# Kernel optimization log

Measured on AMD Instinct MI355X. Metric: run time of the kernel, lower is better.

Reference implementation:

```python
import jax, jax.numpy as jnp
import numpy as np

N_NODES = 100000
N_EDGES = 1600000
IN_DIM = 128
OUT_DIM = 64


def setup_inputs() -> dict:
    key = jax.random.key(0)
    k1, k2, k3 = jax.random.split(key, 3)
    x = jax.random.normal(k1, (N_NODES, IN_DIM), dtype=jnp.float32)
    edge_index = jax.random.randint(k2, (2, N_EDGES), 0, N_NODES, dtype=jnp.int64)
    W = jax.random.normal(k3, (IN_DIM, OUT_DIM), dtype=jnp.float32) * (1.0 / np.sqrt(IN_DIM))
    b = jnp.zeros((OUT_DIM,), dtype=jnp.float32)
    return {"x": x, "edge_index": edge_index, "W": W, "b": b}


def reference(x, edge_index, W, b):
    row = edge_index[0]  # source nodes
    col = edge_index[1]  # target nodes (aggregation index)
    n = x.shape[0]

    # gcn_norm with add_self_loops=False: degree from edge weights (ones) at target
    ones = jnp.ones((edge_index.shape[1],), dtype=x.dtype)
    deg = jax.ops.segment_sum(ones, col, num_segments=n)  # [N]
    deg_inv_sqrt = jnp.where(deg > 0, jax.lax.rsqrt(jnp.maximum(deg, 1e-12)), 0.0)
    norm = deg_inv_sqrt[row] * deg_inv_sqrt[col]  # [E]

    # linear transform first (bias added after aggregation, as in PyG GCNConv)
    h = x @ W  # [N, OUT_DIM]

    # gather source features, scale by norm, scatter-add to targets
    msg = h[row] * norm[:, None]  # [E, OUT_DIM]
    out = jax.ops.segment_sum(msg, col, num_segments=n) + b  # [N, OUT_DIM]

    return jax.nn.relu(out)
```

## Files before the change

kernel.cpp:

```cpp
#include <hip/hip_runtime.h>
#include <hip/hip_bf16.h>

#define IN_DIM 128
#define OUT_DIM 64
#define CLOG 9
#define CNPB (1 << CLOG)
#define FLOG 7
#define FNPB (1 << FLOG)
#define MAXCOARSE 1024
#define B1 256
#define CAP 4096

static inline size_t align_up(size_t v, size_t a) { return (v + a - 1) & ~(a - 1); }

__device__ __forceinline__ unsigned short f2bf(float f) {
    unsigned int x = __float_as_uint(f);
    unsigned int r = (x + 0x7fffu + ((x >> 16) & 1u)) >> 16;
    return (unsigned short)r;
}

typedef _Float16 half8 __attribute__((ext_vector_type(8)));
typedef float f32x4 __attribute__((ext_vector_type(4)));

__global__ void __launch_bounds__(256) kA_ticket(
    const int* __restrict__ col, int* __restrict__ BinTotal,
    int* __restrict__ tickets, int n_edges, int nbuck, int chunk) {
    __shared__ int hist[MAXCOARSE];
    int t = threadIdx.x;
    for (int i = t; i < nbuck; i += 256) hist[i] = 0;
    __syncthreads();
    int start = blockIdx.x * chunk;
    int end = min(n_edges, start + chunk);
    for (int i = start + t; i < end; i += 256)
        atomicAdd(&hist[col[i] >> CLOG], 1);
    __syncthreads();
    int* trow = tickets + (size_t)blockIdx.x * nbuck;
    for (int i = t; i < nbuck; i += 256)
        trow[i] = atomicAdd(&BinTotal[i], hist[i]);
}

__global__ void __launch_bounds__(256) kS2_scantotals(
    const int* __restrict__ BinTotal, int* __restrict__ BucketStart,
    int nbuck, int n_edges) {
    __shared__ int s[256];
    int t = threadIdx.x;
    int v[4];
#pragma unroll
    for (int j = 0; j < 4; ++j) {
        int idx = t * 4 + j;
        v[j] = (idx < nbuck) ? BinTotal[idx] : 0;
    }
    int tsum = v[0] + v[1] + v[2] + v[3];
    s[t] = tsum;
    __syncthreads();
    for (int off = 1; off < 256; off <<= 1) {
        int x = (t >= off) ? s[t - off] : 0;
        __syncthreads();
        s[t] += x;
        __syncthreads();
    }
    int run = s[t] - tsum;
#pragma unroll
    for (int j = 0; j < 4; ++j) {
        int idx = t * 4 + j;
        if (idx < nbuck) BucketStart[idx] = run;
        run += v[j];
    }
    if (t == 0) BucketStart[nbuck] = n_edges;
}

__global__ void __launch_bounds__(256) kB_scatter(
    const int* __restrict__ row, const int* __restrict__ col,
    const int* __restrict__ BucketStart, const int* __restrict__ tickets,
    unsigned int* __restrict__ EdgeBuf, int n_edges, int nbuck, int chunk) {
    __shared__ int cur[MAXCOARSE];
    const int* trow = tickets + (size_t)blockIdx.x * nbuck;
    int t = threadIdx.x;
    for (int i = t; i < nbuck; i += 256)
        cur[i] = BucketStart[i] + trow[i];
    __syncthreads();
    int start = blockIdx.x * chunk;
    int end = min(n_edges, start + chunk);
    for (int i = start + t; i < end; i += 256) {
        int c = col[i];
        int r = row[i];
        int bin = c >> CLOG;
        int p = atomicAdd(&cur[bin], 1);
        EdgeBuf[p] = ((unsigned int)r << CLOG) | (unsigned int)(c & (CNPB - 1));
    }
}

__global__ void __launch_bounds__(256) kD_degree(
    const unsigned int* __restrict__ EdgeBuf, const int* __restrict__ BucketStart,
    float* __restrict__ dis, int n_nodes) {
    __shared__ int cnt[CNPB];
    int t = threadIdx.x;
    for (int i = t; i < CNPB; i += 256) cnt[i] = 0;
    __syncthreads();
    int es = BucketStart[blockIdx.x];
    int ee = BucketStart[blockIdx.x + 1];
    for (int i = es + t; i < ee; i += 256)
        atomicAdd(&cnt[EdgeBuf[i] & (CNPB - 1)], 1);
    __syncthreads();
    int nb0 = blockIdx.x << CLOG;
    for (int i = t; i < CNPB; i += 256) {
        int node = nb0 + i;
        if (node < n_nodes) {
            int d = cnt[i];
            dis[node] = (d > 0) ? rsqrtf((float)d) : 0.0f;
        }
    }
}

__global__ void __launch_bounds__(256) k_matmul_mfma(
    const float* __restrict__ x, const float* __restrict__ W,
    const float* __restrict__ dis, unsigned short* __restrict__ h, int n_nodes) {
    const int lane = threadIdx.x & 63;
    const int m = lane & 15;
    const int q = lane >> 4;
    const int wid = (blockIdx.x * blockDim.x + threadIdx.x) >> 6;
    const int ntiles = (n_nodes + 15) >> 4;
    if (wid >= ntiles) return;

    half8 bfrag[4][4];
#pragma unroll
    for (int kt = 0; kt < 4; ++kt) {
#pragma unroll
        for (int nt = 0; nt < 4; ++nt) {
            int k0 = kt * 32 + q * 8;
            int c = nt * 16 + m;
#pragma unroll
            for (int j = 0; j < 8; ++j)
                bfrag[kt][nt][j] = (_Float16)W[(size_t)(k0 + j) * OUT_DIM + c];
        }
    }

    const int nb = wid << 4;
    int arow = nb + m;
    if (arow >= n_nodes) arow = n_nodes - 1;
    const float* xr = x + (size_t)arow * IN_DIM;

    f32x4 acc[4];
#pragma unroll
    for (int nt = 0; nt < 4; ++nt) acc[nt] = (f32x4){0.f, 0.f, 0.f, 0.f};

#pragma unroll
    for (int kt = 0; kt < 4; ++kt) {
        const float4* xp = (const float4*)(xr + kt * 32 + q * 8);
        float4 lo = xp[0];
        float4 hi = xp[1];
        half8 afrag;
        afrag[0] = (_Float16)lo.x; afrag[1] = (_Float16)lo.y;
        afrag[2] = (_Float16)lo.z; afrag[3] = (_Float16)lo.w;
        afrag[4] = (_Float16)hi.x; afrag[5] = (_Float16)hi.y;
        afrag[6] = (_Float16)hi.z; afrag[7] = (_Float16)hi.w;
#pragma unroll
        for (int nt = 0; nt < 4; ++nt)
            acc[nt] = __builtin_amdgcn_mfma_f32_16x16x32_f16(afrag, bfrag[kt][nt],
                                                             acc[nt], 0, 0, 0);
    }

#pragma unroll
    for (int r = 0; r < 4; ++r) {
        int node = nb + q * 4 + r;
        if (node < n_nodes) {
            float dv = dis[node];
            unsigned short* hp = h + (size_t)node * OUT_DIM + m;
#pragma unroll
            for (int nt = 0; nt < 4; ++nt)
                hp[nt * 16] = f2bf(acc[nt][r] * dv);
        }
    }
}

__global__ void __launch_bounds__(512) kF_sortagg(
    const unsigned int* __restrict__ EdgeBuf, const int* __restrict__ BucketStart,
    const float* __restrict__ dis, const unsigned short* __restrict__ h,
    const float* __restrict__ b, float* __restrict__ out,
    int* __restrict__ spill, int* __restrict__ spillcur, int n_nodes) {
    __shared__ int cnt[FNPB];
    __shared__ int seg[FNPB];
    __shared__ int cursor[FNPB];
    __shared__ int sbuf[CAP];
    __shared__ int sbase_sh;
    int t = threadIdx.x;
    int parent = blockIdx.x >> 2;
    int sub = blockIdx.x & 3;
    int es = BucketStart[parent];
    int ee = BucketStart[parent + 1];
    int nb0 = blockIdx.x << FLOG;

    if (t < FNPB) cnt[t] = 0;
    __syncthreads();
    for (int i = es + t; i < ee; i += 512) {
        unsigned int v = EdgeBuf[i];
        if ((int)((v >> FLOG) & 3u) == sub)
            atomicAdd(&cnt[v & (FNPB - 1)], 1);
    }
    __syncthreads();

    if (t < FNPB) seg[t] = cnt[t];
    __syncthreads();
    for (int off = 1; off < FNPB; off <<= 1) {
        int x = 0;
        if (t < FNPB && t >= off) x = seg[t - off];
        __syncthreads();
        if (t < FNPB) seg[t] += x;
        __syncthreads();
    }
    if (t < FNPB) cursor[t] = seg[t] - cnt[t];
    __syncthreads();

    int ne_f = seg[FNPB - 1];
    if (t == 0 && ne_f > CAP) sbase_sh = atomicAdd(spillcur, ne_f);
    __syncthreads();

    const int lane = t & 63;
    const int wv = t >> 6;
    const int quarter = lane >> 4;
    const int qlane = lane & 15;
    float4 bias = ((const float4*)b)[qlane];

    if (ne_f <= CAP) {
        for (int i = es + t; i < ee; i += 512) {
            unsigned int v = EdgeBuf[i];
            if ((int)((v >> FLOG) & 3u) == sub) {
                int p = atomicAdd(&cursor[v & (FNPB - 1)], 1);
                sbuf[p] = (int)(v >> CLOG);
            }
        }
        __syncthreads();

        for (int nl = wv; nl < FNPB; nl += 8) {
            int node = nb0 + nl;
            if (node >= n_nodes) break;
            int e_ = seg[nl];
            int s_ = e_ - cnt[nl];
            float a0 = 0.f, a1 = 0.f, a2 = 0.f, a3 = 0.f;
            for (int j0 = s_; j0 < e_; j0 += 8) {
                int iA = j0 + quarter;
                int iB = j0 + quarter + 4;
                int rA = sbuf[iA < e_ ? iA : s_];
                int rB = sbuf[iB < e_ ? iB : s_];
                uint2 vA = make_uint2(0u, 0u), vB = make_uint2(0u, 0u);
                if (iA < e_)
                    vA = *(const uint2*)(h + (size_t)rA * OUT_DIM + qlane * 4);
                if (iB < e_)
                    vB = *(const uint2*)(h + (size_t)rB * OUT_DIM + qlane * 4);
                a0 += __uint_as_float(vA.x << 16);
                a1 += __uint_as_float(vA.x & 0xFFFF0000u);
                a2 += __uint_as_float(vA.y << 16);
                a3 += __uint_as_float(vA.y & 0xFFFF0000u);
                a0 += __uint_as_float(vB.x << 16);
                a1 += __uint_as_float(vB.x & 0xFFFF0000u);
                a2 += __uint_as_float(vB.y << 16);
                a3 += __uint_as_float(vB.y & 0xFFFF0000u);
            }
            a0 += __shfl_xor(a0, 16, 64); a0 += __shfl_xor(a0, 32, 64);
            a1 += __shfl_xor(a1, 16, 64); a1 += __shfl_xor(a1, 32, 64);
            a2 += __shfl_xor(a2, 16, 64); a2 += __shfl_xor(a2, 32, 64);
            a3 += __shfl_xor(a3, 16, 64); a3 += __shfl_xor(a3, 32, 64);
            if (quarter == 0) {
                float dv = dis[node];
                float4 o;
                o.x = fmaxf(fmaf(a0, dv, bias.x), 0.f);
                o.y = fmaxf(fmaf(a1, dv, bias.y), 0.f);
                o.z = fmaxf(fmaf(a2, dv, bias.z), 0.f);
                o.w = fmaxf(fmaf(a3, dv, bias.w), 0.f);
                ((float4*)(out + (size_t)node * OUT_DIM))[qlane] = o;
            }
        }
    } else {
        int sbase = sbase_sh;
        for (int i = es + t; i < ee; i += 512) {
            unsigned int v = EdgeBuf[i];
            if ((int)((v >> FLOG) & 3u) == sub) {
                int p = atomicAdd(&cursor[v & (FNPB - 1)], 1);
                spill[sbase + p] = (int)(v >> CLOG);
            }
        }
        __threadfence();
        __syncthreads();
        for (int nl = wv; nl < FNPB; nl += 8) {
            int node = nb0 + nl;
            if (node >= n_nodes) break;
            int e_ = seg[nl];
            int s_ = e_ - cnt[nl];
            float a0 = 0.f, a1 = 0.f, a2 = 0.f, a3 = 0.f;
            for (int j0 = s_; j0 < e_; j0 += 8) {
                int iA = j0 + quarter;
                int iB = j0 + quarter + 4;
                int rA = spill[sbase + (iA < e_ ? iA : s_)];
                int rB = spill[sbase + (iB < e_ ? iB : s_)];
                uint2 vA = make_uint2(0u, 0u), vB = make_uint2(0u, 0u);
                if (iA < e_)
                    vA = *(const uint2*)(h + (size_t)rA * OUT_DIM + qlane * 4);
                if (iB < e_)
                    vB = *(const uint2*)(h + (size_t)rB * OUT_DIM + qlane * 4);
                a0 += __uint_as_float(vA.x << 16);
                a1 += __uint_as_float(vA.x & 0xFFFF0000u);
                a2 += __uint_as_float(vA.y << 16);
                a3 += __uint_as_float(vA.y & 0xFFFF0000u);
                a0 += __uint_as_float(vB.x << 16);
                a1 += __uint_as_float(vB.x & 0xFFFF0000u);
                a2 += __uint_as_float(vB.y << 16);
                a3 += __uint_as_float(vB.y & 0xFFFF0000u);
            }
            a0 += __shfl_xor(a0, 16, 64); a0 += __shfl_xor(a0, 32, 64);
            a1 += __shfl_xor(a1, 16, 64); a1 += __shfl_xor(a1, 32, 64);
            a2 += __shfl_xor(a2, 16, 64); a2 += __shfl_xor(a2, 32, 64);
            a3 += __shfl_xor(a3, 16, 64); a3 += __shfl_xor(a3, 32, 64);
            if (quarter == 0) {
                float dv = dis[node];
                float4 o;
                o.x = fmaxf(fmaf(a0, dv, bias.x), 0.f);
                o.y = fmaxf(fmaf(a1, dv, bias.y), 0.f);
                o.z = fmaxf(fmaf(a2, dv, bias.z), 0.f);
                o.w = fmaxf(fmaf(a3, dv, bias.w), 0.f);
                ((float4*)(out + (size_t)node * OUT_DIM))[qlane] = o;
            }
        }
    }
}

#define MM_NODES 16
__global__ void __launch_bounds__(256) k_matmul_f32(
    const float* __restrict__ x, const float* __restrict__ W,
    const float* __restrict__ dis, float* __restrict__ h, int n_nodes) {
    __shared__ float xs[MM_NODES * IN_DIM];
    const int lane = threadIdx.x & 63;
    const int wv = threadIdx.x >> 6;
    float w[IN_DIM];
#pragma unroll
    for (int k = 0; k < IN_DIM; ++k) w[k] = W[k * OUT_DIM + lane];
    int nchunks = (n_nodes + MM_NODES - 1) / MM_NODES;
    for (int ch = blockIdx.x; ch < nchunks; ch += gridDim.x) {
        int base = ch * MM_NODES;
        int nrows = min(MM_NODES, n_nodes - base);
        __syncthreads();
        const float4* xg = (const float4*)(x + (size_t)base * IN_DIM);
        int nf4 = nrows * IN_DIM / 4;
        for (int i = threadIdx.x; i < nf4; i += 256) ((float4*)xs)[i] = xg[i];
        __syncthreads();
#pragma unroll
        for (int j = 0; j < 4; ++j) {
            int local = wv * 4 + j;
            int node = base + local;
            if (local < nrows) {
                const float4* xr = (const float4*)(xs + local * IN_DIM);
                float acc = 0.0f;
#pragma unroll
                for (int k4 = 0; k4 < IN_DIM / 4; ++k4) {
                    float4 xv = xr[k4];
                    acc = fmaf(xv.x, w[k4 * 4 + 0], acc);
                    acc = fmaf(xv.y, w[k4 * 4 + 1], acc);
                    acc = fmaf(xv.z, w[k4 * 4 + 2], acc);
                    acc = fmaf(xv.w, w[k4 * 4 + 3], acc);
                }
                h[(size_t)node * OUT_DIM + lane] = acc * dis[node];
            }
        }
    }
}

__global__ void k_degree_fb(const int* __restrict__ col, int* __restrict__ deg,
                            int n_edges) {
    int i = blockIdx.x * blockDim.x + threadIdx.x;
    int stride = gridDim.x * blockDim.x;
    for (; i < n_edges; i += stride) atomicAdd(&deg[col[i]], 1);
}

__global__ void k_rsqrt_fb(const int* __restrict__ deg, float* __restrict__ dis, int n) {
    int i = blockIdx.x * blockDim.x + threadIdx.x;
    if (i < n) {
        int d = deg[i];
        dis[i] = (d > 0) ? rsqrtf((float)d) : 0.0f;
    }
}

__global__ void __launch_bounds__(256) k_scatter_fb(
    const int* __restrict__ row, const int* __restrict__ col,
    const float* __restrict__ dis, const float* __restrict__ h,
    float* __restrict__ out, int n_edges) {
    const int lane = threadIdx.x & 63;
    int e = (blockIdx.x * blockDim.x + threadIdx.x) >> 6;
    int nw = (gridDim.x * blockDim.x) >> 6;
    for (; e < n_edges; e += nw) {
        int r = row[e];
        int c = col[e];
        float v = h[(size_t)r * OUT_DIM + lane] * dis[c];
        atomicAdd(&out[(size_t)c * OUT_DIM + lane], v);
    }
}

__global__ void k_bias_relu_fb(float* __restrict__ out, const float* __restrict__ b,
                               int total) {
    int i = blockIdx.x * blockDim.x + threadIdx.x;
    int stride = gridDim.x * blockDim.x;
    for (; i < total; i += stride) {
        float v = out[i] + b[i & (OUT_DIM - 1)];
        out[i] = fmaxf(v, 0.0f);
    }
}

extern "C" void kernel_launch(void* const* d_in, const int* in_sizes, int n_in,
                              void* d_out, int out_size, void* d_ws, size_t ws_size,
                              hipStream_t stream) {
    const float* x = (const float*)d_in[0];
    const int* ei = (const int*)d_in[1];
    const float* W = (const float*)d_in[2];
    const float* b = (const float*)d_in[3];
    float* out = (float*)d_out;

    const int n_nodes = in_sizes[0] / IN_DIM;
    const int n_edges = in_sizes[1] / 2;
    const int* row = ei;
    const int* col = ei + n_edges;

    const int nbc = (n_nodes + CNPB - 1) >> CLOG;
    const int nbf = (n_nodes + FNPB - 1) >> FLOG;
    const int chunk = (n_edges + B1 - 1) / B1;

    char* wsb = (char*)d_ws;
    size_t off = 0;
    int* BinTotal = (int*)(wsb + off);   off += align_up((size_t)(nbc + 8) * 4, 256);
    int* spillcur = BinTotal + nbc;
    int* BucketStart = (int*)(wsb + off);off += align_up((size_t)(nbc + 1) * 4, 256);
    int* tickets = (int*)(wsb + off);    off += align_up((size_t)B1 * nbc * 4, 256);
    float* dis = (float*)(wsb + off);    off += align_up((size_t)n_nodes * 4, 256);
    unsigned int* EdgeBuf = (unsigned int*)(wsb + off);
                                         off += align_up((size_t)n_edges * 4, 256);
    int* spill = (int*)(wsb + off);      off += align_up((size_t)n_edges * 4, 256);
    unsigned short* h = (unsigned short*)(wsb + off);
                                         off += (size_t)n_nodes * OUT_DIM * 2;
    const size_t needed = off;

    const bool ok = (ws_size >= needed) && (nbc <= MAXCOARSE) &&
                    (n_nodes <= (1 << 22));

    if (ok) {
        hipMemsetAsync(BinTotal, 0, (size_t)(nbc + 8) * 4, stream);
        kA_ticket<<<B1, 256, 0, stream>>>(col, BinTotal, tickets, n_edges, nbc,
                                          chunk);
        kS2_scantotals<<<1, 256, 0, stream>>>(BinTotal, BucketStart, nbc, n_edges);
        kB_scatter<<<B1, 256, 0, stream>>>(row, col, BucketStart, tickets, EdgeBuf,
                                           n_edges, nbc, chunk);
        kD_degree<<<nbc, 256, 0, stream>>>(EdgeBuf, BucketStart, dis, n_nodes);
        int ntiles = (n_nodes + 15) / 16;
        int mm_blocks = (ntiles + 3) / 4;
        k_matmul_mfma<<<mm_blocks, 256, 0, stream>>>(x, W, dis, h, n_nodes);
        kF_sortagg<<<nbf, 512, 0, stream>>>(EdgeBuf, BucketStart, dis, h, b,
                                            out, spill, spillcur, n_nodes);
    } else {
        char* p = (char*)d_ws;
        int* deg_f = (int*)p;
        float* dis_f = (float*)(p + align_up((size_t)n_nodes * 4, 256));
        float* h_f = (float*)(p + 2 * align_up((size_t)n_nodes * 4, 256));
        hipMemsetAsync(deg_f, 0, (size_t)n_nodes * 4, stream);
        hipMemsetAsync(out, 0, (size_t)out_size * 4, stream);
        k_degree_fb<<<1024, 256, 0, stream>>>(col, deg_f, n_edges);
        k_rsqrt_fb<<<(n_nodes + 255) / 256, 256, 0, stream>>>(deg_f, dis_f, n_nodes);
        k_matmul_f32<<<1024, 256, 0, stream>>>(x, W, dis_f, h_f, n_nodes);
        k_scatter_fb<<<2048, 256, 0, stream>>>(row, col, dis_f, h_f, out, n_edges);
        k_bias_relu_fb<<<2048, 256, 0, stream>>>(out, b, n_nodes * OUT_DIM);
    }
}
```

Before: 193.3 us.

## Fuse edge bucketing passes into one cooperative kernel with fine buckets

Replaces the ticket/scan/scatter/degree kernel sequence with a single cooperative kernel that uses grid-wide syncs, keeping per-block bucket offsets in shared memory instead of a global tickets array. It also switches from coarse 512-node buckets to fine 128-node buckets directly, so the aggregation kernel no longer rescans a parent bucket four times and filters by sub-bucket. The costs are grid-sync overhead, a redundant scan done by every block, and a dependence on cooperative launch support, with the multi-kernel path kept as a fallback.

```diff
diff --git a/kernel.cpp b/kernel.cpp
--- a/kernel.cpp
+++ b/kernel.cpp
@@ -1,14 +1,15 @@
 #include <hip/hip_runtime.h>
 #include <hip/hip_bf16.h>
+#include <hip/hip_cooperative_groups.h>
+
+namespace cg = cooperative_groups;
 
 #define IN_DIM 128
 #define OUT_DIM 64
-#define CLOG 9
-#define CNPB (1 << CLOG)
 #define FLOG 7
 #define FNPB (1 << FLOG)
-#define MAXCOARSE 1024
-#define B1 256
+#define MAXFINE 1024
+#define GB 256
 #define CAP 4096
 
 static inline size_t align_up(size_t v, size_t a) { return (v + a - 1) & ~(a - 1); }
@@ -22,33 +23,112 @@
 typedef _Float16 half8 __attribute__((ext_vector_type(8)));
 typedef float f32x4 __attribute__((ext_vector_type(4)));
 
-__global__ void __launch_bounds__(256) kA_ticket(
+__global__ void __launch_bounds__(256) kBuild(
+    const int* __restrict__ row, const int* __restrict__ col,
+    int* __restrict__ BinTotal, int* __restrict__ BucketStart,
+    unsigned int* __restrict__ EdgeBuf, float* __restrict__ dis,
+    int n_nodes, int n_edges, int nbf, int chunk) {
+    __shared__ int hist[MAXFINE];
+    __shared__ int bs[MAXFINE];
+    __shared__ int s[256];
+    __shared__ int cnt[FNPB];
+    int t = threadIdx.x;
+    int start = blockIdx.x * chunk;
+    int end = min(n_edges, start + chunk);
+
+    for (int i = t; i < nbf; i += 256) hist[i] = 0;
+    __syncthreads();
+    for (int i = start + t; i < end; i += 256)
+        atomicAdd(&hist[col[i] >> FLOG], 1);
+    __syncthreads();
+    for (int i = t; i < nbf; i += 256)
+        hist[i] = atomicAdd(&BinTotal[i], hist[i]);
+
+    cg::this_grid().sync();
+
+    int v[4];
+#pragma unroll
+    for (int j = 0; j < 4; ++j) {
+        int idx = t * 4 + j;
+        v[j] = (idx < nbf) ? BinTotal[idx] : 0;
+    }
+    int tsum = v[0] + v[1] + v[2] + v[3];
+    s[t] = tsum;
+    __syncthreads();
+    for (int off = 1; off < 256; off <<= 1) {
+        int x = (t >= off) ? s[t - off] : 0;
+        __syncthreads();
+        s[t] += x;
+        __syncthreads();
+    }
+    int run = s[t] - tsum;
+#pragma unroll
+    for (int j = 0; j < 4; ++j) {
+        int idx = t * 4 + j;
+        if (idx < nbf) {
+            bs[idx] = run;
+            if (blockIdx.x == 0) BucketStart[idx] = run;
+        }
+        run += v[j];
+    }
+    if (blockIdx.x == 0 && t == 0) BucketStart[nbf] = n_edges;
+    __syncthreads();
+    for (int i = t; i < nbf; i += 256) hist[i] += bs[i];
+    __syncthreads();
+
+    for (int i = start + t; i < end; i += 256) {
+        int c = col[i];
+        int r = row[i];
+        int p = atomicAdd(&hist[c >> FLOG], 1);
+        EdgeBuf[p] = ((unsigned int)r << FLOG) | (unsigned int)(c & (FNPB - 1));
+    }
+
+    cg::this_grid().sync();
+
+    for (int b = blockIdx.x; b < nbf; b += GB) {
+        int es = bs[b];
+        int ee = (b + 1 < nbf) ? bs[b + 1] : n_edges;
+        if (t < FNPB) cnt[t] = 0;
+        __syncthreads();
+        for (int i = es + t; i < ee; i += 256)
+            atomicAdd(&cnt[EdgeBuf[i] & (FNPB - 1)], 1);
+        __syncthreads();
+        int node = (b << FLOG) + t;
+        if (t < FNPB && node < n_nodes) {
+            int d = cnt[t];
+            dis[node] = (d > 0) ? rsqrtf((float)d) : 0.0f;
+        }
+        __syncthreads();
+    }
+}
+
+__global__ void __launch_bounds__(256) kP1_ticket(
     const int* __restrict__ col, int* __restrict__ BinTotal,
-    int* __restrict__ tickets, int n_edges, int nbuck, int chunk) {
-    __shared__ int hist[MAXCOARSE];
+    int* __restrict__ tickets, int n_edges, int nbf, int chunk) {
+    __shared__ int hist[MAXFINE];
     int t = threadIdx.x;
-    for (int i = t; i < nbuck; i += 256) hist[i] = 0;
+    for (int i = t; i < nbf; i += 256) hist[i] = 0;
     __syncthreads();
     int start = blockIdx.x * chunk;
     int end = min(n_edges, start + chunk);
     for (int i = start + t; i < end; i += 256)
-        atomicAdd(&hist[col[i] >> CLOG], 1);
-    __syncthreads();
-    int* trow = tickets + (size_t)blockIdx.x * nbuck;
-    for (int i = t; i < nbuck; i += 256)
+        atomicAdd(&hist[col[i] >> FLOG], 1);
+    __syncthreads();
+    int* trow = tickets + (size_t)blockIdx.x * nbf;
+    for (int i = t; i < nbf; i += 256)
         trow[i] = atomicAdd(&BinTotal[i], hist[i]);
 }
 
-__global__ void __launch_bounds__(256) kS2_scantotals(
+__global__ void __launch_bounds__(256) kP2_scan(
     const int* __restrict__ BinTotal, int* __restrict__ BucketStart,
-    int nbuck, int n_edges) {
+    int nbf, int n_edges) {
     __shared__ int s[256];
     int t = threadIdx.x;
     int v[4];
 #pragma unroll
     for (int j = 0; j < 4; ++j) {
         int idx = t * 4 + j;
-        v[j] = (idx < nbuck) ? BinTotal[idx] : 0;
+        v[j] = (idx < nbf) ? BinTotal[idx] : 0;
     }
     int tsum = v[0] + v[1] + v[2] + v[3];
     s[t] = tsum;
@@ -63,20 +143,20 @@
 #pragma unroll
     for (int j = 0; j < 4; ++j) {
         int idx = t * 4 + j;
-        if (idx < nbuck) BucketStart[idx] = run;
+        if (idx < nbf) BucketStart[idx] = run;
         run += v[j];
     }
-    if (t == 0) BucketStart[nbuck] = n_edges;
-}
-
-__global__ void __launch_bounds__(256) kB_scatter(
+    if (t == 0) BucketStart[nbf] = n_edges;
+}
+
+__global__ void __launch_bounds__(256) kP3_scatter(
     const int* __restrict__ row, const int* __restrict__ col,
     const int* __restrict__ BucketStart, const int* __restrict__ tickets,
-    unsigned int* __restrict__ EdgeBuf, int n_edges, int nbuck, int chunk) {
-    __shared__ int cur[MAXCOARSE];
-    const int* trow = tickets + (size_t)blockIdx.x * nbuck;
+    unsigned int* __restrict__ EdgeBuf, int n_edges, int nbf, int chunk) {
+    __shared__ int cur[MAXFINE];
+    const int* trow = tickets + (size_t)blockIdx.x * nbf;
     int t = threadIdx.x;
-    for (int i = t; i < nbuck; i += 256)
+    for (int i = t; i < nbf; i += 256)
         cur[i] = BucketStart[i] + trow[i];
     __syncthreads();
     int start = blockIdx.x * chunk;
@@ -84,31 +164,27 @@
     for (int i = start + t; i < end; i += 256) {
         int c = col[i];
         int r = row[i];
-        int bin = c >> CLOG;
-        int p = atomicAdd(&cur[bin], 1);
-        EdgeBuf[p] = ((unsigned int)r << CLOG) | (unsigned int)(c & (CNPB - 1));
-    }
-}
-
-__global__ void __launch_bounds__(256) kD_degree(
+        int p = atomicAdd(&cur[c >> FLOG], 1);
+        EdgeBuf[p] = ((unsigned int)r << FLOG) | (unsigned int)(c & (FNPB - 1));
+    }
+}
+
+__global__ void __launch_bounds__(256) kP4_degree(
     const unsigned int* __restrict__ EdgeBuf, const int* __restrict__ BucketStart,
     float* __restrict__ dis, int n_nodes) {
-    __shared__ int cnt[CNPB];
+    __shared__ int cnt[FNPB];
     int t = threadIdx.x;
-    for (int i = t; i < CNPB; i += 256) cnt[i] = 0;
+    if (t < FNPB) cnt[t] = 0;
     __syncthreads();
     int es = BucketStart[blockIdx.x];
     int ee = BucketStart[blockIdx.x + 1];
     for (int i = es + t; i < ee; i += 256)
-        atomicAdd(&cnt[EdgeBuf[i] & (CNPB - 1)], 1);
-    __syncthreads();
-    int nb0 = blockIdx.x << CLOG;
-    for (int i = t; i < CNPB; i += 256) {
-        int node = nb0 + i;
-        if (node < n_nodes) {
-            int d = cnt[i];
-            dis[node] = (d > 0) ? rsqrtf((float)d) : 0.0f;
-        }
+        atomicAdd(&cnt[EdgeBuf[i] & (FNPB - 1)], 1);
+    __syncthreads();
+    int node = (blockIdx.x << FLOG) + t;
+    if (t < FNPB && node < n_nodes) {
+        int d = cnt[t];
+        dis[node] = (d > 0) ? rsqrtf((float)d) : 0.0f;
     }
 }
 
@@ -184,19 +260,15 @@
     __shared__ int sbuf[CAP];
     __shared__ int sbase_sh;
     int t = threadIdx.x;
-    int parent = blockIdx.x >> 2;
-    int sub = blockIdx.x & 3;
-    int es = BucketStart[parent];
-    int ee = BucketStart[parent + 1];
+    int es = BucketStart[blockIdx.x];
+    int ee = BucketStart[blockIdx.x + 1];
+    int ne = ee - es;
     int nb0 = blockIdx.x << FLOG;
 
     if (t < FNPB) cnt[t] = 0;
     __syncthreads();
-    for (int i = es + t; i < ee; i += 512) {
-        unsigned int v = EdgeBuf[i];
-        if ((int)((v >> FLOG) & 3u) == sub)
-            atomicAdd(&cnt[v & (FNPB - 1)], 1);
-    }
+    for (int i = es + t; i < ee; i += 512)
+        atomicAdd(&cnt[EdgeBuf[i] & (FNPB - 1)], 1);
     __syncthreads();
 
     if (t < FNPB) seg[t] = cnt[t];
@@ -211,8 +283,7 @@
     if (t < FNPB) cursor[t] = seg[t] - cnt[t];
     __syncthreads();
 
-    int ne_f = seg[FNPB - 1];
-    if (t == 0 && ne_f > CAP) sbase_sh = atomicAdd(spillcur, ne_f);
+    if (t == 0 && ne > CAP) sbase_sh = atomicAdd(spillcur, ne);
     __syncthreads();
 
     const int lane = t & 63;
@@ -221,13 +292,11 @@
     const int qlane = lane & 15;
     float4 bias = ((const float4*)b)[qlane];
 
-    if (ne_f <= CAP) {
+    if (ne <= CAP) {
         for (int i = es + t; i < ee; i += 512) {
             unsigned int v = EdgeBuf[i];
-            if ((int)((v >> FLOG) & 3u) == sub) {
-                int p = atomicAdd(&cursor[v & (FNPB - 1)], 1);
-                sbuf[p] = (int)(v >> CLOG);
-            }
+            int p = atomicAdd(&cursor[v & (FNPB - 1)], 1);
+            sbuf[p] = (int)(v >> FLOG);
         }
         __syncthreads();
 
@@ -274,10 +343,8 @@
         int sbase = sbase_sh;
         for (int i = es + t; i < ee; i += 512) {
             unsigned int v = EdgeBuf[i];
-            if ((int)((v >> FLOG) & 3u) == sub) {
-                int p = atomicAdd(&cursor[v & (FNPB - 1)], 1);
-                spill[sbase + p] = (int)(v >> CLOG);
-            }
+            int p = atomicAdd(&cursor[v & (FNPB - 1)], 1);
+            spill[sbase + p] = (int)(v >> FLOG);
         }
         __threadfence();
         __syncthreads();
@@ -417,16 +484,15 @@
     const int* row = ei;
     const int* col = ei + n_edges;
 
-    const int nbc = (n_nodes + CNPB - 1) >> CLOG;
     const int nbf = (n_nodes + FNPB - 1) >> FLOG;
-    const int chunk = (n_edges + B1 - 1) / B1;
+    const int chunk = (n_edges + GB - 1) / GB;
 
     char* wsb = (char*)d_ws;
     size_t off = 0;
-    int* BinTotal = (int*)(wsb + off);   off += align_up((size_t)(nbc + 8) * 4, 256);
-    int* spillcur = BinTotal + nbc;
-    int* BucketStart = (int*)(wsb + off);off += align_up((size_t)(nbc + 1) * 4, 256);
-    int* tickets = (int*)(wsb + off);    off += align_up((size_t)B1 * nbc * 4, 256);
+    int* BinTotal = (int*)(wsb + off);   off += align_up((size_t)(nbf + 8) * 4, 256);
+    int* spillcur = BinTotal + nbf;
+    int* BucketStart = (int*)(wsb + off);off += align_up((size_t)(nbf + 1) * 4, 256);
+    int* tickets = (int*)(wsb + off);    off += align_up((size_t)GB * nbf * 4, 256);
     float* dis = (float*)(wsb + off);    off += align_up((size_t)n_nodes * 4, 256);
     unsigned int* EdgeBuf = (unsigned int*)(wsb + off);
                                          off += align_up((size_t)n_edges * 4, 256);
@@ -435,17 +501,36 @@
                                          off += (size_t)n_nodes * OUT_DIM * 2;
     const size_t needed = off;
 
-    const bool ok = (ws_size >= needed) && (nbc <= MAXCOARSE) &&
-                    (n_nodes <= (1 << 22));
+    const bool ok = (ws_size >= needed) && (nbf <= MAXFINE) &&
+                    (n_nodes <= (1 << 24));
 
     if (ok) {
-        hipMemsetAsync(BinTotal, 0, (size_t)(nbc + 8) * 4, stream);
-        kA_ticket<<<B1, 256, 0, stream>>>(col, BinTotal, tickets, n_edges, nbc,
-                                          chunk);
-        kS2_scantotals<<<1, 256, 0, stream>>>(BinTotal, BucketStart, nbc, n_edges);
-        kB_scatter<<<B1, 256, 0, stream>>>(row, col, BucketStart, tickets, EdgeBuf,
-                                           n_edges, nbc, chunk);
-        kD_degree<<<nbc, 256, 0, stream>>>(EdgeBuf, BucketStart, dis, n_nodes);
+        int coop = 0;
+        int dev = 0;
+        hipGetDevice(&dev);
+        hipDeviceGetAttribute(&coop, hipDeviceAttributeCooperativeLaunch, dev);
+
+        hipMemsetAsync(BinTotal, 0, (size_t)(nbf + 8) * 4, stream);
+        if (coop) {
+            const int* row_a = row;
+            const int* col_a = col;
+            int* bt_a = BinTotal;
+            int* bs_a = BucketStart;
+            unsigned int* eb_a = EdgeBuf;
+            float* dis_a = dis;
+            int nn_a = n_nodes, ne_a = n_edges, nbf_a = nbf, ch_a = chunk;
+            void* args[] = {&row_a, &col_a, &bt_a, &bs_a, &eb_a, &dis_a,
+                            &nn_a, &ne_a, &nbf_a, &ch_a};
+            hipLaunchCooperativeKernel((const void*)kBuild, dim3(GB), dim3(256),
+                                       args, 0, stream);
+        } else {
+            kP1_ticket<<<GB, 256, 0, stream>>>(col, BinTotal, tickets, n_edges,
+                                               nbf, chunk);
+            kP2_scan<<<1, 256, 0, stream>>>(BinTotal, BucketStart, nbf, n_edges);
+            kP3_scatter<<<GB, 256, 0, stream>>>(row, col, BucketStart, tickets,
+                                                EdgeBuf, n_edges, nbf, chunk);
+            kP4_degree<<<nbf, 256, 0, stream>>>(EdgeBuf, BucketStart, dis, n_nodes);
+        }
         int ntiles = (n_nodes + 15) / 16;
         int mm_blocks = (ntiles + 3) / 4;
         k_matmul_mfma<<<mm_blocks, 256, 0, stream>>>(x, W, dis, h, n_nodes);
```

Result: slower. 266.2 us (+37.7%).

## Bucket edges directly at fine granularity and fold degree into ticket pass

Applied to the files above, without the earlier changes.

Replaces the two-level coarse/fine bucketing with a single fine-grained (128-node) bucket sort, so the aggregation kernel no longer filters edges by sub-bucket and each edge is read once per block. Degree counting moves into the ticket kernel via global atomics, which removes the separate degree kernel and the dis array; rsqrt is recomputed from counts in the matmul and aggregation kernels. The ticket and scatter passes now use 512 blocks of 512 threads. The cost is a larger tickets table, 1.6M global atomics on deg, and more buckets per histogram.

```diff
diff --git a/kernel.cpp b/kernel.cpp
--- a/kernel.cpp
+++ b/kernel.cpp
@@ -3,12 +3,11 @@
 
 #define IN_DIM 128
 #define OUT_DIM 64
-#define CLOG 9
-#define CNPB (1 << CLOG)
 #define FLOG 7
 #define FNPB (1 << FLOG)
-#define MAXCOARSE 1024
-#define B1 256
+#define MAXFINE 1024
+#define BB 512
+#define BT 512
 #define CAP 4096
 
 static inline size_t align_up(size_t v, size_t a) { return (v + a - 1) & ~(a - 1); }
@@ -22,33 +21,37 @@
 typedef _Float16 half8 __attribute__((ext_vector_type(8)));
 typedef float f32x4 __attribute__((ext_vector_type(4)));
 
-__global__ void __launch_bounds__(256) kA_ticket(
+__global__ void __launch_bounds__(BT) kA_ticket(
     const int* __restrict__ col, int* __restrict__ BinTotal,
-    int* __restrict__ tickets, int n_edges, int nbuck, int chunk) {
-    __shared__ int hist[MAXCOARSE];
+    int* __restrict__ deg, int* __restrict__ tickets,
+    int n_edges, int nbf, int chunk) {
+    __shared__ int hist[MAXFINE];
     int t = threadIdx.x;
-    for (int i = t; i < nbuck; i += 256) hist[i] = 0;
+    for (int i = t; i < nbf; i += BT) hist[i] = 0;
     __syncthreads();
     int start = blockIdx.x * chunk;
     int end = min(n_edges, start + chunk);
-    for (int i = start + t; i < end; i += 256)
-        atomicAdd(&hist[col[i] >> CLOG], 1);
-    __syncthreads();
-    int* trow = tickets + (size_t)blockIdx.x * nbuck;
-    for (int i = t; i < nbuck; i += 256)
+    for (int i = start + t; i < end; i += BT) {
+        int c = col[i];
+        atomicAdd(&hist[c >> FLOG], 1);
+        atomicAdd(&deg[c], 1);
+    }
+    __syncthreads();
+    int* trow = tickets + (size_t)blockIdx.x * nbf;
+    for (int i = t; i < nbf; i += BT)
         trow[i] = atomicAdd(&BinTotal[i], hist[i]);
 }
 
 __global__ void __launch_bounds__(256) kS2_scantotals(
     const int* __restrict__ BinTotal, int* __restrict__ BucketStart,
-    int nbuck, int n_edges) {
+    int nbf, int n_edges) {
     __shared__ int s[256];
     int t = threadIdx.x;
     int v[4];
 #pragma unroll
     for (int j = 0; j < 4; ++j) {
         int idx = t * 4 + j;
-        v[j] = (idx < nbuck) ? BinTotal[idx] : 0;
+        v[j] = (idx < nbf) ? BinTotal[idx] : 0;
     }
     int tsum = v[0] + v[1] + v[2] + v[3];
     s[t] = tsum;
@@ -63,58 +66,35 @@
 #pragma unroll
     for (int j = 0; j < 4; ++j) {
         int idx = t * 4 + j;
-        if (idx < nbuck) BucketStart[idx] = run;
+        if (idx < nbf) BucketStart[idx] = run;
         run += v[j];
     }
-    if (t == 0) BucketStart[nbuck] = n_edges;
-}
-
-__global__ void __launch_bounds__(256) kB_scatter(
+    if (t == 0) BucketStart[nbf] = n_edges;
+}
+
+__global__ void __launch_bounds__(BT) kB_scatter(
     const int* __restrict__ row, const int* __restrict__ col,
     const int* __restrict__ BucketStart, const int* __restrict__ tickets,
-    unsigned int* __restrict__ EdgeBuf, int n_edges, int nbuck, int chunk) {
-    __shared__ int cur[MAXCOARSE];
-    const int* trow = tickets + (size_t)blockIdx.x * nbuck;
+    unsigned int* __restrict__ EdgeBuf, int n_edges, int nbf, int chunk) {
+    __shared__ int cur[MAXFINE];
+    const int* trow = tickets + (size_t)blockIdx.x * nbf;
     int t = threadIdx.x;
-    for (int i = t; i < nbuck; i += 256)
+    for (int i = t; i < nbf; i += BT)
         cur[i] = BucketStart[i] + trow[i];
     __syncthreads();
     int start = blockIdx.x * chunk;
     int end = min(n_edges, start + chunk);
-    for (int i = start + t; i < end; i += 256) {
+    for (int i = start + t; i < end; i += BT) {
         int c = col[i];
         int r = row[i];
-        int bin = c >> CLOG;
-        int p = atomicAdd(&cur[bin], 1);
-        EdgeBuf[p] = ((unsigned int)r << CLOG) | (unsigned int)(c & (CNPB - 1));
-    }
-}
-
-__global__ void __launch_bounds__(256) kD_degree(
-    const unsigned int* __restrict__ EdgeBuf, const int* __restrict__ BucketStart,
-    float* __restrict__ dis, int n_nodes) {
-    __shared__ int cnt[CNPB];
-    int t = threadIdx.x;
-    for (int i = t; i < CNPB; i += 256) cnt[i] = 0;
-    __syncthreads();
-    int es = BucketStart[blockIdx.x];
-    int ee = BucketStart[blockIdx.x + 1];
-    for (int i = es + t; i < ee; i += 256)
-        atomicAdd(&cnt[EdgeBuf[i] & (CNPB - 1)], 1);
-    __syncthreads();
-    int nb0 = blockIdx.x << CLOG;
-    for (int i = t; i < CNPB; i += 256) {
-        int node = nb0 + i;
-        if (node < n_nodes) {
-            int d = cnt[i];
-            dis[node] = (d > 0) ? rsqrtf((float)d) : 0.0f;
-        }
+        int p = atomicAdd(&cur[c >> FLOG], 1);
+        EdgeBuf[p] = ((unsigned int)r << FLOG) | (unsigned int)(c & (FNPB - 1));
     }
 }
 
 __global__ void __launch_bounds__(256) k_matmul_mfma(
     const float* __restrict__ x, const float* __restrict__ W,
-    const float* __restrict__ dis, unsigned short* __restrict__ h, int n_nodes) {
+    const int* __restrict__ deg, unsigned short* __restrict__ h, int n_nodes) {
     const int lane = threadIdx.x & 63;
     const int m = lane & 15;
     const int q = lane >> 4;
@@ -164,7 +144,8 @@
     for (int r = 0; r < 4; ++r) {
         int node = nb + q * 4 + r;
         if (node < n_nodes) {
-            float dv = dis[node];
+            int d = deg[node];
+            float dv = (d > 0) ? rsqrtf((float)d) : 0.0f;
             unsigned short* hp = h + (size_t)node * OUT_DIM + m;
 #pragma unroll
             for (int nt = 0; nt < 4; ++nt)
@@ -175,28 +156,24 @@
 
 __global__ void __launch_bounds__(512) kF_sortagg(
     const unsigned int* __restrict__ EdgeBuf, const int* __restrict__ BucketStart,
-    const float* __restrict__ dis, const unsigned short* __restrict__ h,
-    const float* __restrict__ b, float* __restrict__ out,
-    int* __restrict__ spill, int* __restrict__ spillcur, int n_nodes) {
+    const unsigned short* __restrict__ h, const float* __restrict__ b,
+    float* __restrict__ out, int* __restrict__ spill, int* __restrict__ spillcur,
+    int n_nodes) {
     __shared__ int cnt[FNPB];
     __shared__ int seg[FNPB];
     __shared__ int cursor[FNPB];
     __shared__ int sbuf[CAP];
     __shared__ int sbase_sh;
     int t = threadIdx.x;
-    int parent = blockIdx.x >> 2;
-    int sub = blockIdx.x & 3;
-    int es = BucketStart[parent];
-    int ee = BucketStart[parent + 1];
+    int es = BucketStart[blockIdx.x];
+    int ee = BucketStart[blockIdx.x + 1];
+    int ne = ee - es;
     int nb0 = blockIdx.x << FLOG;
 
     if (t < FNPB) cnt[t] = 0;
     __syncthreads();
-    for (int i = es + t; i < ee; i += 512) {
-        unsigned int v = EdgeBuf[i];
-        if ((int)((v >> FLOG) & 3u) == sub)
-            atomicAdd(&cnt[v & (FNPB - 1)], 1);
-    }
+    for (int i = es + t; i < ee; i += 512)
+        atomicAdd(&cnt[EdgeBuf[i] & (FNPB - 1)], 1);
     __syncthreads();
 
     if (t < FNPB) seg[t] = cnt[t];
@@ -211,8 +188,7 @@
     if (t < FNPB) cursor[t] = seg[t] - cnt[t];
     __syncthreads();
 
-    int ne_f = seg[FNPB - 1];
-    if (t == 0 && ne_f > CAP) sbase_sh = atomicAdd(spillcur, ne_f);
+    if (t == 0 && ne > CAP) sbase_sh = atomicAdd(spillcur, ne);
     __syncthreads();
 
     const int lane = t & 63;
@@ -221,13 +197,11 @@
     const int qlane = lane & 15;
     float4 bias = ((const float4*)b)[qlane];
 
-    if (ne_f <= CAP) {
+    if (ne <= CAP) {
         for (int i = es + t; i < ee; i += 512) {
             unsigned int v = EdgeBuf[i];
-            if ((int)((v >> FLOG) & 3u) == sub) {
-                int p = atomicAdd(&cursor[v & (FNPB - 1)], 1);
-                sbuf[p] = (int)(v >> CLOG);
-            }
+            int p = atomicAdd(&cursor[v & (FNPB - 1)], 1);
+            sbuf[p] = (int)(v >> FLOG);
         }
         __syncthreads();
 
@@ -235,7 +209,8 @@
             int node = nb0 + nl;
             if (node >= n_nodes) break;
             int e_ = seg[nl];
-            int s_ = e_ - cnt[nl];
+            int dcount = cnt[nl];
+            int s_ = e_ - dcount;
             float a0 = 0.f, a1 = 0.f, a2 = 0.f, a3 = 0.f;
             for (int j0 = s_; j0 < e_; j0 += 8) {
                 int iA = j0 + quarter;
@@ -261,7 +236,7 @@
             a2 += __shfl_xor(a2, 16, 64); a2 += __shfl_xor(a2, 32, 64);
             a3 += __shfl_xor(a3, 16, 64); a3 += __shfl_xor(a3, 32, 64);
             if (quarter == 0) {
-                float dv = dis[node];
+                float dv = (dcount > 0) ? rsqrtf((float)dcount) : 0.0f;
                 float4 o;
                 o.x = fmaxf(fmaf(a0, dv, bias.x), 0.f);
                 o.y = fmaxf(fmaf(a1, dv, bias.y), 0.f);
@@ -274,10 +249,8 @@
         int sbase = sbase_sh;
         for (int i = es + t; i < ee; i += 512) {
             unsigned int v = EdgeBuf[i];
-            if ((int)((v >> FLOG) & 3u) == sub) {
-                int p = atomicAdd(&cursor[v & (FNPB - 1)], 1);
-                spill[sbase + p] = (int)(v >> CLOG);
-            }
+            int p = atomicAdd(&cursor[v & (FNPB - 1)], 1);
+            spill[sbase + p] = (int)(v >> FLOG);
         }
         __threadfence();
         __syncthreads();
@@ -285,7 +258,8 @@
             int node = nb0 + nl;
             if (node >= n_nodes) break;
             int e_ = seg[nl];
-            int s_ = e_ - cnt[nl];
+            int dcount = cnt[nl];
+            int s_ = e_ - dcount;
             float a0 = 0.f, a1 = 0.f, a2 = 0.f, a3 = 0.f;
             for (int j0 = s_; j0 < e_; j0 += 8) {
                 int iA = j0 + quarter;
@@ -311,7 +285,7 @@
             a2 += __shfl_xor(a2, 16, 64); a2 += __shfl_xor(a2, 32, 64);
             a3 += __shfl_xor(a3, 16, 64); a3 += __shfl_xor(a3, 32, 64);
             if (quarter == 0) {
-                float dv = dis[node];
+                float dv = (dcount > 0) ? rsqrtf((float)dcount) : 0.0f;
                 float4 o;
                 o.x = fmaxf(fmaf(a0, dv, bias.x), 0.f);
                 o.y = fmaxf(fmaf(a1, dv, bias.y), 0.f);
@@ -417,17 +391,18 @@
     const int* row = ei;
     const int* col = ei + n_edges;
 
-    const int nbc = (n_nodes + CNPB - 1) >> CLOG;
     const int nbf = (n_nodes + FNPB - 1) >> FLOG;
-    const int chunk = (n_edges + B1 - 1) / B1;
+    const int chunk = (n_edges + BB - 1) / BB;
 
     char* wsb = (char*)d_ws;
     size_t off = 0;
-    int* BinTotal = (int*)(wsb + off);   off += align_up((size_t)(nbc + 8) * 4, 256);
-    int* spillcur = BinTotal + nbc;
-    int* BucketStart = (int*)(wsb + off);off += align_up((size_t)(nbc + 1) * 4, 256);
-    int* tickets = (int*)(wsb + off);    off += align_up((size_t)B1 * nbc * 4, 256);
-    float* dis = (float*)(wsb + off);    off += align_up((size_t)n_nodes * 4, 256);
+    int* BinTotal = (int*)(wsb + off);   off += (size_t)(nbf + 8) * 4;
+    int* spillcur = BinTotal + nbf;
+    int* deg = (int*)(wsb + off);        off += (size_t)n_nodes * 4;
+    const size_t zero_bytes = off;
+    off = align_up(off, 256);
+    int* BucketStart = (int*)(wsb + off);off += align_up((size_t)(nbf + 1) * 4, 256);
+    int* tickets = (int*)(wsb + off);    off += align_up((size_t)BB * nbf * 4, 256);
     unsigned int* EdgeBuf = (unsigned int*)(wsb + off);
                                          off += align_up((size_t)n_edges * 4, 256);
     int* spill = (int*)(wsb + off);      off += align_up((size_t)n_edges * 4, 256);
@@ -435,22 +410,21 @@
                                          off += (size_t)n_nodes * OUT_DIM * 2;
     const size_t needed = off;
 
-    const bool ok = (ws_size >= needed) && (nbc <= MAXCOARSE) &&
-                    (n_nodes <= (1 << 22));
+    const bool ok = (ws_size >= needed) && (nbf <= MAXFINE) &&
+                    (n_nodes <= (1 << 24));
 
     if (ok) {
-        hipMemsetAsync(BinTotal, 0, (size_t)(nbc + 8) * 4, stream);
-        kA_ticket<<<B1, 256, 0, stream>>>(col, BinTotal, tickets, n_edges, nbc,
-                                          chunk);
-        kS2_scantotals<<<1, 256, 0, stream>>>(BinTotal, BucketStart, nbc, n_edges);
-        kB_scatter<<<B1, 256, 0, stream>>>(row, col, BucketStart, tickets, EdgeBuf,
-                                           n_edges, nbc, chunk);
-        kD_degree<<<nbc, 256, 0, stream>>>(EdgeBuf, BucketStart, dis, n_nodes);
+        hipMemsetAsync(BinTotal, 0, zero_bytes, stream);
+        kA_ticket<<<BB, BT, 0, stream>>>(col, BinTotal, deg, tickets, n_edges,
+                                         nbf, chunk);
+        kS2_scantotals<<<1, 256, 0, stream>>>(BinTotal, BucketStart, nbf, n_edges);
+        kB_scatter<<<BB, BT, 0, stream>>>(row, col, BucketStart, tickets, EdgeBuf,
+                                          n_edges, nbf, chunk);
         int ntiles = (n_nodes + 15) / 16;
         int mm_blocks = (ntiles + 3) / 4;
-        k_matmul_mfma<<<mm_blocks, 256, 0, stream>>>(x, W, dis, h, n_nodes);
-        kF_sortagg<<<nbf, 512, 0, stream>>>(EdgeBuf, BucketStart, dis, h, b,
-                                            out, spill, spillcur, n_nodes);
+        k_matmul_mfma<<<mm_blocks, 256, 0, stream>>>(x, W, deg, h, n_nodes);
+        kF_sortagg<<<nbf, 512, 0, stream>>>(EdgeBuf, BucketStart, h, b, out,
+                                            spill, spillcur, n_nodes);
     } else {
         char* p = (char*)d_ws;
         int* deg_f = (int*)p;
```

After: 241.9 us. +25.2%, slower.
